# Optimization experiments

Measured on AMD Instinct MI355X. Metric: run time of the kernel, lower is better.

## Reference

```python
import jax, jax.numpy as jnp
import numpy as np

MIN_BIN_WIDTH = 1e-3
MIN_BIN_HEIGHT = 1e-3
MIN_DERIVATIVE = 1e-3
TAIL_BOUND = 1.0
N_POS = 2097152
N_CHANNELS = 8
N_BINS = 128
DEFAULT_INIT = float(np.log(np.exp(1.0 - MIN_DERIVATIVE) - 1.0))


def setup_inputs() -> dict:
    key = jax.random.key(0)
    k1, k2, k3, k4 = jax.random.split(key, 4)
    # positions rescaled to roughly [-1, 1]; include slight tail overshoot
    x = jax.random.uniform(k1, (N_POS, N_CHANNELS), minval=-1.1, maxval=1.1, dtype=jnp.float32)
    uw = DEFAULT_INIT + 0.1 * jax.random.normal(k2, (N_CHANNELS, N_BINS), dtype=jnp.float32)
    uh = DEFAULT_INIT + 0.1 * jax.random.normal(k3, (N_CHANNELS, N_BINS), dtype=jnp.float32)
    ud = DEFAULT_INIT + 0.1 * jax.random.normal(k4, (N_CHANNELS, N_BINS - 1), dtype=jnp.float32)
    return {"x": x, "unnormalized_widths": uw, "unnormalized_heights": uh,
            "unnormalized_derivatives": ud}


def _bin_edges(unnormalized, min_size, left, right):
    # softmax-normalized sizes with a minimum bin size, cumsum -> knot locations
    n_bins = unnormalized.shape[-1]
    sizes = jax.nn.softmax(unnormalized, axis=-1)
    sizes = min_size + (1.0 - min_size * n_bins) * sizes
    cum = jnp.cumsum(sizes, axis=-1)
    cum = jnp.pad(cum, ((0, 0), (1, 0)))
    cum = (right - left) * cum + left
    cum = cum.at[..., 0].set(left).at[..., -1].set(right)
    sizes = cum[..., 1:] - cum[..., :-1]
    return sizes, cum


def _log_prob(x, uw, uh, ud):
    left, right = -TAIL_BOUND, TAIL_BOUND
    bottom, top = -TAIL_BOUND, TAIL_BOUND
    C = uw.shape[0]

    widths, cumwidths = _bin_edges(uw * 10.0, MIN_BIN_WIDTH, left, right)      # (C,B),(C,B+1)
    heights, cumheights = _bin_edges(uh * 10.0, MIN_BIN_HEIGHT, bottom, top)   # (C,B),(C,B+1)
    ud_pad = jnp.pad(ud, ((0, 0), (1, 1)), constant_values=DEFAULT_INIT)       # linear tails
    derivatives = MIN_DERIVATIVE + jax.nn.softplus(ud_pad)                      # (C,B+1)
    delta = heights / widths                                                    # (C,B)

    inside = (x >= left) & (x <= right)
    xc = jnp.clip(x, bottom, top)  # inverse pass searches over cumheights

    edges = cumheights.at[:, -1].add(1e-6)
    # per-channel bin search, memory-light searchsorted
    idx = jax.vmap(lambda e, v: jnp.searchsorted(e, v, side='right'),
                   in_axes=(0, 1), out_axes=1)(edges, xc) - 1                   # (N,C)
    idx = jnp.clip(idx, 0, widths.shape[-1] - 1)

    ch = jnp.arange(C)[None, :]
    icw = cumwidths[ch, idx]
    ibw = widths[ch, idx]
    ich = cumheights[ch, idx]
    ih = heights[ch, idx]
    idl = delta[ch, idx]
    d0 = derivatives[ch, idx]
    d1 = derivatives[ch, idx + 1]

    # quadratic inverse solve (Durkan et al. rational-quadratic spline)
    dy = xc - ich
    t = d0 + d1 - 2.0 * idl
    a = dy * t + ih * (idl - d0)
    b = ih * d0 - dy * t
    c = -idl * dy
    disc = jnp.maximum(b * b - 4.0 * a * c, 0.0)
    root = (2.0 * c) / (-b - jnp.sqrt(disc))
    theta_1m = root * (1.0 - root)
    denom = idl + t * theta_1m
    der_num = (idl ** 2) * (d1 * root ** 2 + 2.0 * idl * theta_1m + d0 * (1.0 - root) ** 2)
    logabsdet = jnp.log(der_num) - 2.0 * jnp.log(denom)
    logdet = jnp.where(inside, -logabsdet, 0.0)  # identity tails -> logdet 0
    return np.log(0.5).astype(np.float32) + logdet


def reference(x, unnormalized_widths, unnormalized_heights, unnormalized_derivatives):
    return _log_prob(x, unnormalized_widths, unnormalized_heights, unnormalized_derivatives)
```

## Files before the change

### kernel.cpp

```cpp
#include <hip/hip_runtime.h>
#include <math.h>


#define NB 128
#define NCH 8
#define NSLOT 1024
#define HINT_B 20640
#define TAB_FLOATS 9256

static __device__ inline unsigned f2h(float v) {
    union { _Float16 h; unsigned short u; } c;
    c.h = (_Float16)v;
    return (unsigned)c.u;
}
static __device__ inline float h16lo(unsigned u) {
    union { unsigned short s; _Float16 h; } c; c.s = (unsigned short)(u & 0xffffu);
    return (float)c.h;
}
static __device__ inline float h16hi(unsigned u) {
    union { unsigned short s; _Float16 h; } c; c.s = (unsigned short)(u >> 16);
    return (float)c.h;
}

__global__ __launch_bounds__(128) void spline_precompute(
    const float* __restrict__ uw, const float* __restrict__ uh,
    const float* __restrict__ ud, float* __restrict__ ws)
{
    const int c = blockIdx.x;
    const int i = threadIdx.x;
    __shared__ float red[128];
    __shared__ float scan[128];
    __shared__ float cum[129];
    __shared__ float wdt[128];
    __shared__ float sdv[129];
    const float DEFAULT_INIT = logf(expf(1.0f - 1e-3f) - 1.0f);

    float v = uw[c * NB + i] * 10.0f;
    red[i] = v; __syncthreads();
    #pragma unroll
    for (int s = 64; s >= 1; s >>= 1) { if (i < s) red[i] = fmaxf(red[i], red[i + s]); __syncthreads(); }
    float ex = expf(v - red[0]);
    __syncthreads();
    red[i] = ex; __syncthreads();
    #pragma unroll
    for (int s = 64; s >= 1; s >>= 1) { if (i < s) red[i] += red[i + s]; __syncthreads(); }
    float sz = 1e-3f + (1.0f - 1e-3f * NB) * (ex / red[0]);
    __syncthreads();
    scan[i] = sz;
    for (int off = 1; off < NB; off <<= 1) {
        __syncthreads();
        float t = (i >= off) ? scan[i - off] : 0.0f;
        __syncthreads();
        scan[i] += t;
    }
    __syncthreads();
    if (i == 0) cum[0] = -1.0f;
    cum[i + 1] = (i == NB - 1) ? 1.0f : fmaf(2.0f, scan[i], -1.0f);
    __syncthreads();
    wdt[i] = cum[i + 1] - cum[i];
    __syncthreads();

    v = uh[c * NB + i] * 10.0f;
    red[i] = v; __syncthreads();
    #pragma unroll
    for (int s = 64; s >= 1; s >>= 1) { if (i < s) red[i] = fmaxf(red[i], red[i + s]); __syncthreads(); }
    ex = expf(v - red[0]);
    __syncthreads();
    red[i] = ex; __syncthreads();
    #pragma unroll
    for (int s = 64; s >= 1; s >>= 1) { if (i < s) red[i] += red[i + s]; __syncthreads(); }
    sz = 1e-3f + (1.0f - 1e-3f * NB) * (ex / red[0]);
    __syncthreads();
    scan[i] = sz;
    for (int off = 1; off < NB; off <<= 1) {
        __syncthreads();
        float t = (i >= off) ? scan[i - off] : 0.0f;
        __syncthreads();
        scan[i] += t;
    }
    __syncthreads();
    if (i == 0) cum[0] = -1.0f;
    cum[i + 1] = (i == NB - 1) ? 1.0f : fmaf(2.0f, scan[i], -1.0f);

    float u0 = (i == 0) ? DEFAULT_INIT : ud[c * (NB - 1) + i - 1];
    sdv[i] = 1e-3f + log1pf(expf(u0));
    if (i == NB - 1) sdv[NB] = 1e-3f + log1pf(expf(DEFAULT_INIT));
    __syncthreads();

    float hh  = cum[i + 1] - cum[i];
    float idl = hh / wdt[i];
    float d0v = sdv[i], d1v = sdv[i + 1];
    float Tv  = d0v + d1v - 2.0f * idl;

    unsigned* g_rec = reinterpret_cast<unsigned*>(ws);
    const int rw = (c * 129 + i) * 5;
    g_rec[rw]     = __float_as_uint(cum[i]);
    g_rec[rw + 1] = __float_as_uint(hh);
    g_rec[rw + 2] = f2h(idl) | (f2h(d0v) << 16);
    g_rec[rw + 3] = f2h(Tv);
    g_rec[rw + 4] = 0u;
    if (i == NB - 1) {
        const int pw = (c * 129 + NB) * 5;
        g_rec[pw]     = __float_as_uint(1.0f);
        g_rec[pw + 1] = __float_as_uint(1.0f);
        g_rec[pw + 2] = f2h(1.0f) | (f2h(1.0f) << 16);
        g_rec[pw + 3] = 0u;
        g_rec[pw + 4] = 0u;
    }

    unsigned short* g_hint = reinterpret_cast<unsigned short*>(
        reinterpret_cast<char*>(ws) + HINT_B);
    for (int s = i; s < NSLOT; s += NB) {
        float left = (float)s * (2.0f / NSLOT) - 1.0f;
        int k = 0;
        #pragma unroll
        for (int st = 64; st >= 1; st >>= 1) {
            int t = k + st;
            if (cum[t] <= left) k = t;
        }
        float X = (cum[k + 1] - left) * 262144.0f;
        int split = (int)ceilf(X) - 1;
        split = split < 0 ? 0 : (split > 511 ? 511 : split);
        g_hint[c * NSLOT + s] = (unsigned short)(k | (split << 7));
    }
}

__global__ __launch_bounds__(256, 4) void spline_main(
    const float4* __restrict__ x4, float4* __restrict__ out4,
    const float* __restrict__ ws, int npair)
{
    __shared__ __align__(16) float tab[TAB_FLOATS];
    {
        float4* dst = reinterpret_cast<float4*>(tab);
        const float4* src = reinterpret_cast<const float4*>(ws);
        for (int t = threadIdx.x; t < TAB_FLOATS / 4; t += 256) dst[t] = src[t];
    }
    __syncthreads();
    const unsigned* rec = reinterpret_cast<const unsigned*>(tab);
    const unsigned short* hint = reinterpret_cast<const unsigned short*>(
        reinterpret_cast<const char*>(tab) + HINT_B);

    const float LOG_HALF = -0.6931471805599453f;
    const float LN2 = 0.6931471805599453f;
    const int tid = blockIdx.x * 256 + threadIdx.x;
    const int stride = gridDim.x * 256;

    float4 pfa, pfb;
    if (tid < npair) { pfa = x4[2 * tid]; pfb = x4[2 * tid + 1]; }

    for (int i = tid; i < npair; i += stride) {
        float4 xa = pfa, xb = pfb;
        int inx = i + stride;
        inx = (inx < npair) ? inx : i;
        pfa = x4[2 * inx];
        pfb = x4[2 * inx + 1];

        float xs[8] = {xa.x, xa.y, xa.z, xa.w, xb.x, xb.y, xb.z, xb.w};
        float rs[8];

        #pragma unroll
        for (int j = 0; j < 8; ++j) {
            float xin = xs[j];
            float xc = __builtin_amdgcn_fmed3f(xin, -1.0f, 1.0f);
            float g = fmaf(xc, 262144.0f, 262144.0f);
            int gi = (int)g;
            gi = gi > 524287 ? 524287 : gi;
            int q = gi & 511;
            unsigned hv = hint[j * NSLOT + (gi >> 9)];
            int k2 = (int)(hv & 127u) + ((q > (int)(hv >> 7)) ? 1 : 0);

            const unsigned* p = rec + (j * 129 + k2) * 5;
            float e_lo = __uint_as_float(p[0]);
            float h    = __uint_as_float(p[1]);
            unsigned w2 = p[2];
            float T    = h16lo(p[3]);
            float dl = h16lo(w2), d0 = h16hi(w2);

            float dy  = __builtin_amdgcn_fmed3f(xc - e_lo, 0.0f, h);
            float dyt = dy * T;
            float a   = fmaf(h, dl - d0, dyt);
            float b   = fmaf(h, d0, -dyt);
            float cp  = dl * dy;
            float a4  = 4.0f * a;
            float disc = fmaxf(fmaf(a4, cp, b * b), 0.0f);
            float sq  = __builtin_amdgcn_sqrtf(disc);
            float t2  = b + sq;
            float uu  = cp + cp;
            float t2s = t2 * t2;
            float denb = fmaf(T * uu, t2 - uu, dl * t2s);
            float numf = h * denb;
            float den  = (dl * sq) * t2s;
            float la = __log2f(numf) - __log2f(den);
            float lm = (xin == xc) ? LN2 : 0.0f;
            rs[j] = fmaf(lm, la, LOG_HALF);
        }

        out4[2 * i]     = make_float4(rs[0], rs[1], rs[2], rs[3]);
        out4[2 * i + 1] = make_float4(rs[4], rs[5], rs[6], rs[7]);
    }
}

extern "C" void kernel_launch(void* const* d_in, const int* in_sizes, int n_in,
                              void* d_out, int out_size, void* d_ws, size_t ws_size,
                              hipStream_t stream) {
    const float* x  = (const float*)d_in[0];
    const float* uw = (const float*)d_in[1];
    const float* uh = (const float*)d_in[2];
    const float* ud = (const float*)d_in[3];
    float* ws = (float*)d_ws;

    spline_precompute<<<NCH, NB, 0, stream>>>(uw, uh, ud, ws);

    const int npair = out_size / 8;
    spline_main<<<2048, 256, 0, stream>>>(
        (const float4*)x, (float4*)d_out, ws, npair);
}
```

Baseline: 41.24 us.

## Pack spline records into 16-byte uint4 and rewrite precompute with wave shuffles

Each per-bin record shrinks from five 32-bit words to four, stored as a uint4, so the main kernel fetches a record with one 128-bit LDS read instead of several scalar reads, and the shared table copy gets smaller. The precompute kernel now runs as a single 64-lane wavefront handling two bins per lane, using shuffle-based max, sum and scan instead of shared-memory trees with many barriers. This cuts setup latency, but the cumulative sums are formed differently, which can slightly change the edge values.

```diff
diff --git a/kernel.cpp b/kernel.cpp
--- a/kernel.cpp
+++ b/kernel.cpp
@@ -5,8 +5,8 @@
 #define NB 128
 #define NCH 8
 #define NSLOT 1024
-#define HINT_B 20640
-#define TAB_FLOATS 9256
+#define HINT_B 16512
+#define TAB_FLOATS 8224
 
 static __device__ inline unsigned f2h(float v) {
     union { _Float16 h; unsigned short u; } c;
@@ -22,103 +22,99 @@
     return (float)c.h;
 }
 
-__global__ __launch_bounds__(128) void spline_precompute(
+__global__ __launch_bounds__(64) void spline_precompute(
     const float* __restrict__ uw, const float* __restrict__ uh,
     const float* __restrict__ ud, float* __restrict__ ws)
 {
     const int c = blockIdx.x;
-    const int i = threadIdx.x;
-    __shared__ float red[128];
-    __shared__ float scan[128];
-    __shared__ float cum[129];
-    __shared__ float wdt[128];
-    __shared__ float sdv[129];
-    const float DEFAULT_INIT = logf(expf(1.0f - 1e-3f) - 1.0f);
-
-    float v = uw[c * NB + i] * 10.0f;
-    red[i] = v; __syncthreads();
-    #pragma unroll
-    for (int s = 64; s >= 1; s >>= 1) { if (i < s) red[i] = fmaxf(red[i], red[i + s]); __syncthreads(); }
-    float ex = expf(v - red[0]);
+    const int l = threadIdx.x;
+    const int i0 = 2 * l, i1 = i0 + 1;
+    const float DEF = logf(expf(1.0f - 1e-3f) - 1.0f);
+    const float DSP = 1e-3f + log1pf(expf(DEF));
+
+    float a0 = uw[c * NB + i0] * 10.0f, a1 = uw[c * NB + i1] * 10.0f;
+    float mw = fmaxf(a0, a1);
+    #pragma unroll
+    for (int off = 1; off < 64; off <<= 1) mw = fmaxf(mw, __shfl_xor(mw, off, 64));
+    float ew0 = expf(a0 - mw), ew1 = expf(a1 - mw);
+    float sw = ew0 + ew1;
+    #pragma unroll
+    for (int off = 1; off < 64; off <<= 1) sw += __shfl_xor(sw, off, 64);
+    float rw = 1.0f / sw;
+    float zw0 = fmaf(0.872f * ew0, rw, 1e-3f);
+    float zw1 = fmaf(0.872f * ew1, rw, 1e-3f);
+    float tw = zw0 + zw1, Iw = tw;
+    #pragma unroll
+    for (int off = 1; off < 64; off <<= 1) {
+        float u = __shfl_up(Iw, off, 64);
+        if (l >= off) Iw += u;
+    }
+    float Ew = Iw - tw;
+    float cw1 = Ew + zw0;
+    float w0 = 2.0f * zw0;
+    float w1 = (i1 == NB - 1) ? 2.0f * (1.0f - cw1) : 2.0f * zw1;
+
+    float b0 = uh[c * NB + i0] * 10.0f, b1 = uh[c * NB + i1] * 10.0f;
+    float mh = fmaxf(b0, b1);
+    #pragma unroll
+    for (int off = 1; off < 64; off <<= 1) mh = fmaxf(mh, __shfl_xor(mh, off, 64));
+    float eh0 = expf(b0 - mh), eh1 = expf(b1 - mh);
+    float sh = eh0 + eh1;
+    #pragma unroll
+    for (int off = 1; off < 64; off <<= 1) sh += __shfl_xor(sh, off, 64);
+    float rh = 1.0f / sh;
+    float zh0 = fmaf(0.872f * eh0, rh, 1e-3f);
+    float zh1 = fmaf(0.872f * eh1, rh, 1e-3f);
+    float th = zh0 + zh1, Ih = th;
+    #pragma unroll
+    for (int off = 1; off < 64; off <<= 1) {
+        float u = __shfl_up(Ih, off, 64);
+        if (l >= off) Ih += u;
+    }
+    float Eh = Ih - th;
+    float ch1 = Eh + zh0;
+    float elo0 = fmaf(2.0f, Eh, -1.0f);
+    float elo1 = fmaf(2.0f, ch1, -1.0f);
+    float h0 = 2.0f * zh0;
+    float h1 = (i1 == NB - 1) ? 2.0f * (1.0f - ch1) : 2.0f * zh1;
+
+    float du0 = (i0 == 0) ? DEF : ud[c * (NB - 1) + i0 - 1];
+    float du1 = ud[c * (NB - 1) + i1 - 1];
+    float s0 = 1e-3f + log1pf(expf(du0));
+    float s1 = 1e-3f + log1pf(expf(du1));
+    float s2 = __shfl_down(s0, 1, 64);
+    if (l == 63) s2 = DSP;
+
+    float dl0 = h0 / w0, dl1 = h1 / w1;
+    float T0 = s0 + s1 - 2.0f * dl0;
+    float T1 = s1 + s2 - 2.0f * dl1;
+
+    uint4* g_rec = reinterpret_cast<uint4*>(ws);
+    g_rec[c * 129 + i0] = make_uint4(__float_as_uint(elo0), __float_as_uint(h0),
+                                     f2h(dl0) | (f2h(s0) << 16), f2h(T0));
+    g_rec[c * 129 + i1] = make_uint4(__float_as_uint(elo1), __float_as_uint(h1),
+                                     f2h(dl1) | (f2h(s1) << 16), f2h(T1));
+    if (l == 63)
+        g_rec[c * 129 + 128] = make_uint4(__float_as_uint(1.0f), __float_as_uint(1.0f),
+                                          f2h(1.0f) | (f2h(1.0f) << 16), 0u);
+
+    __shared__ float kn[129];
+    kn[i0] = elo0;
+    kn[i1] = elo1;
+    if (l == 63) kn[128] = 1.0f;
     __syncthreads();
-    red[i] = ex; __syncthreads();
-    #pragma unroll
-    for (int s = 64; s >= 1; s >>= 1) { if (i < s) red[i] += red[i + s]; __syncthreads(); }
-    float sz = 1e-3f + (1.0f - 1e-3f * NB) * (ex / red[0]);
-    __syncthreads();
-    scan[i] = sz;
-    for (int off = 1; off < NB; off <<= 1) {
-        __syncthreads();
-        float t = (i >= off) ? scan[i - off] : 0.0f;
-        __syncthreads();
-        scan[i] += t;
-    }
-    __syncthreads();
-    if (i == 0) cum[0] = -1.0f;
-    cum[i + 1] = (i == NB - 1) ? 1.0f : fmaf(2.0f, scan[i], -1.0f);
-    __syncthreads();
-    wdt[i] = cum[i + 1] - cum[i];
-    __syncthreads();
-
-    v = uh[c * NB + i] * 10.0f;
-    red[i] = v; __syncthreads();
-    #pragma unroll
-    for (int s = 64; s >= 1; s >>= 1) { if (i < s) red[i] = fmaxf(red[i], red[i + s]); __syncthreads(); }
-    ex = expf(v - red[0]);
-    __syncthreads();
-    red[i] = ex; __syncthreads();
-    #pragma unroll
-    for (int s = 64; s >= 1; s >>= 1) { if (i < s) red[i] += red[i + s]; __syncthreads(); }
-    sz = 1e-3f + (1.0f - 1e-3f * NB) * (ex / red[0]);
-    __syncthreads();
-    scan[i] = sz;
-    for (int off = 1; off < NB; off <<= 1) {
-        __syncthreads();
-        float t = (i >= off) ? scan[i - off] : 0.0f;
-        __syncthreads();
-        scan[i] += t;
-    }
-    __syncthreads();
-    if (i == 0) cum[0] = -1.0f;
-    cum[i + 1] = (i == NB - 1) ? 1.0f : fmaf(2.0f, scan[i], -1.0f);
-
-    float u0 = (i == 0) ? DEFAULT_INIT : ud[c * (NB - 1) + i - 1];
-    sdv[i] = 1e-3f + log1pf(expf(u0));
-    if (i == NB - 1) sdv[NB] = 1e-3f + log1pf(expf(DEFAULT_INIT));
-    __syncthreads();
-
-    float hh  = cum[i + 1] - cum[i];
-    float idl = hh / wdt[i];
-    float d0v = sdv[i], d1v = sdv[i + 1];
-    float Tv  = d0v + d1v - 2.0f * idl;
-
-    unsigned* g_rec = reinterpret_cast<unsigned*>(ws);
-    const int rw = (c * 129 + i) * 5;
-    g_rec[rw]     = __float_as_uint(cum[i]);
-    g_rec[rw + 1] = __float_as_uint(hh);
-    g_rec[rw + 2] = f2h(idl) | (f2h(d0v) << 16);
-    g_rec[rw + 3] = f2h(Tv);
-    g_rec[rw + 4] = 0u;
-    if (i == NB - 1) {
-        const int pw = (c * 129 + NB) * 5;
-        g_rec[pw]     = __float_as_uint(1.0f);
-        g_rec[pw + 1] = __float_as_uint(1.0f);
-        g_rec[pw + 2] = f2h(1.0f) | (f2h(1.0f) << 16);
-        g_rec[pw + 3] = 0u;
-        g_rec[pw + 4] = 0u;
-    }
 
     unsigned short* g_hint = reinterpret_cast<unsigned short*>(
         reinterpret_cast<char*>(ws) + HINT_B);
-    for (int s = i; s < NSLOT; s += NB) {
+    for (int s = l; s < NSLOT; s += 64) {
         float left = (float)s * (2.0f / NSLOT) - 1.0f;
         int k = 0;
         #pragma unroll
         for (int st = 64; st >= 1; st >>= 1) {
             int t = k + st;
-            if (cum[t] <= left) k = t;
+            if (kn[t] <= left) k = t;
         }
-        float X = (cum[k + 1] - left) * 262144.0f;
+        float X = (kn[k + 1] - left) * 262144.0f;
         int split = (int)ceilf(X) - 1;
         split = split < 0 ? 0 : (split > 511 ? 511 : split);
         g_hint[c * NSLOT + s] = (unsigned short)(k | (split << 7));
@@ -136,7 +132,7 @@
         for (int t = threadIdx.x; t < TAB_FLOATS / 4; t += 256) dst[t] = src[t];
     }
     __syncthreads();
-    const unsigned* rec = reinterpret_cast<const unsigned*>(tab);
+    const uint4* rp = reinterpret_cast<const uint4*>(tab);
     const unsigned short* hint = reinterpret_cast<const unsigned short*>(
         reinterpret_cast<const char*>(tab) + HINT_B);
 
@@ -169,12 +165,11 @@
             unsigned hv = hint[j * NSLOT + (gi >> 9)];
             int k2 = (int)(hv & 127u) + ((q > (int)(hv >> 7)) ? 1 : 0);
 
-            const unsigned* p = rec + (j * 129 + k2) * 5;
-            float e_lo = __uint_as_float(p[0]);
-            float h    = __uint_as_float(p[1]);
-            unsigned w2 = p[2];
-            float T    = h16lo(p[3]);
-            float dl = h16lo(w2), d0 = h16hi(w2);
+            uint4 pr = rp[j * 129 + k2];
+            float e_lo = __uint_as_float(pr.x);
+            float h    = __uint_as_float(pr.y);
+            float dl = h16lo(pr.z), d0 = h16hi(pr.z);
+            float T  = h16lo(pr.w);
 
             float dy  = __builtin_amdgcn_fmed3f(xc - e_lo, 0.0f, h);
             float dyt = dy * T;
@@ -209,7 +204,7 @@
     const float* ud = (const float*)d_in[3];
     float* ws = (float*)d_ws;
 
-    spline_precompute<<<NCH, NB, 0, stream>>>(uw, uh, ud, ws);
+    spline_precompute<<<NCH, 64, 0, stream>>>(uw, uh, ud, ws);
 
     const int npair = out_size / 8;
     spline_main<<<2048, 256, 0, stream>>>(
```

Result: faster. 39.98 us (-3.1%).
